# Kernel optimization log

Measured on AMD Instinct MI355X. Metric: run time of the kernel, lower is better.

## Reference

```python
import jax, jax.numpy as jnp
import numpy as np

NUM_CLASSES = 256
WEIGHT = 0.0005
EPS = 1e-12  # torch F.normalize eps


def setup_inputs() -> dict:
    key = jax.random.key(0)
    k1, k2 = jax.random.split(key)
    features = jax.random.normal(k1, (32768, 1024), dtype=jnp.float32)
    labels = jax.random.randint(k2, (32768,), 0, NUM_CLASSES, dtype=jnp.int32)
    return {"features": features, "labels": labels}


def _centroid_loss(features, labels):
    B, D = features.shape
    # row-wise L2 normalize (torch F.normalize: x / max(||x||, eps))
    norms = jnp.linalg.norm(features, axis=1, keepdims=True)
    f = features / jnp.maximum(norms, EPS)

    ones = jnp.ones((B,), f.dtype)
    counts = jax.ops.segment_sum(ones, labels, num_segments=NUM_CLASSES)  # [C]
    sums = jax.ops.segment_sum(f, labels, num_segments=NUM_CLASSES)       # [C, D]

    # rank of each sample within its class (order of first appearance),
    # matching the row order of features[class_mask] in the original loop
    onehot = jax.nn.one_hot(labels, NUM_CLASSES, dtype=jnp.int32)          # [B, C]
    rank = jnp.take_along_axis(jnp.cumsum(onehot, axis=0), labels[:, None].astype(jnp.int32), axis=1)[:, 0] - 1

    # idx_table[c, r] = global index of the r-th member of class c; sentinel B if none
    idx_table = jnp.full((NUM_CLASSES, B), B, dtype=jnp.int32)
    idx_table = idx_table.at[labels, rank].set(jnp.arange(B, dtype=jnp.int32))

    # NOTE: the original code indexes class_features with the GLOBAL index i
    # (arange(n_c) != i), i.e. it excludes the member of the class at position i,
    # and excludes nothing when i >= n_c. We reproduce that exactly.
    arange_b = jnp.arange(B)
    k = idx_table[labels, arange_b]            # class member at in-class position i (global i)
    valid_excl = k < B                          # exclusion only happens when i < class size
    excl_feat = jnp.where(valid_excl[:, None], f[jnp.where(valid_excl, k, 0)], 0.0)

    n_c = counts[labels]                        # class size per sample (float)
    denom = jnp.where(valid_excl, n_c - 1.0, n_c)
    denom = jnp.maximum(denom, 1.0)             # safe for masked-out singleton classes
    centroid = (sums[labels] - excl_feat) / denom[:, None]

    dist = jnp.mean((f - centroid) ** 2, axis=1)  # F.mse_loss(..., reduction='mean')
    contrib = jnp.where(n_c > 1.0, dist, 0.0)     # skip classes with <=1 sample
    return WEIGHT * jnp.sum(contrib) / B


def reference(features, labels):
    return _centroid_loss(features, labels)
```

## Files before the change

### kernel.cpp

```cpp
#include <hip/hip_runtime.h>

#define BN 32768
#define DN 1024
#define CN 256
#define RCAP 512
#define SUBS 8

__device__ __forceinline__ float dot4(float4 a, float4 b) {
    return a.x*b.x + a.y*b.y + a.z*b.z + a.w*b.w;
}

__global__ void __launch_bounds__(256) kc_compact(const int* __restrict__ labels,
                                                  int* __restrict__ idx,
                                                  int* __restrict__ counts) {
    __shared__ unsigned int packed[BN / 4];
    __shared__ int wcnt[4];
    const int c = blockIdx.x;
    const int t = threadIdx.x;

    for (int w = t; w < BN / 4; w += 256) {
        const int4 v = ((const int4*)labels)[w];
        packed[w] = (unsigned int)(v.x & 255)
                  | ((unsigned int)(v.y & 255) << 8)
                  | ((unsigned int)(v.z & 255) << 16)
                  | ((unsigned int)(v.w & 255) << 24);
    }
    __syncthreads();

    const int wave = t >> 6, lane = t & 63;
    const unsigned long long lt = (lane == 0) ? 0ull : (~0ull >> (64 - lane));
    const int ch0 = wave * 128, ch1 = ch0 + 128;

    int cnt = 0;
    for (int ch = ch0; ch < ch1; ++ch) {
        const int gi = ch * 64 + lane;
        const int lab = (packed[gi >> 2] >> ((gi & 3) * 8)) & 255;
        cnt += __popcll(__ballot(lab == c));
    }
    if (lane == 0) wcnt[wave] = cnt;
    __syncthreads();

    int base = 0;
    for (int w2 = 0; w2 < wave; ++w2) base += wcnt[w2];

    for (int ch = ch0; ch < ch1; ++ch) {
        const int gi = ch * 64 + lane;
        const int lab = (packed[gi >> 2] >> ((gi & 3) * 8)) & 255;
        const bool pred = (lab == c);
        const unsigned long long mask = __ballot(pred);
        if (pred) {
            const int pos = base + __popcll(mask & lt);
            if (pos < RCAP) idx[c * RCAP + pos] = gi;
        }
        base += __popcll(mask);
    }
    if (t == 0) counts[c] = wcnt[0] + wcnt[1] + wcnt[2] + wcnt[3];
}

__global__ void __launch_bounds__(256) k_rnorm(const float4* __restrict__ x4,
                                               float* __restrict__ rnorm) {
    const int wave = threadIdx.x >> 6;
    const int lane = threadIdx.x & 63;
    const int row = blockIdx.x * 4 + wave;
    const float4* base = x4 + (size_t)row * (DN / 4);
    const float4 v0 = base[lane];
    const float4 v1 = base[lane + 64];
    const float4 v2 = base[lane + 128];
    const float4 v3 = base[lane + 192];
    float ss = dot4(v0, v0) + dot4(v1, v1) + dot4(v2, v2) + dot4(v3, v3);
#pragma unroll
    for (int off = 32; off; off >>= 1) ss += __shfl_xor(ss, off, 64);
    if (lane == 0) rnorm[row] = 1.0f / fmaxf(sqrtf(ss), 1e-12f);
}

__global__ void __launch_bounds__(256) k_gather2(const float4* __restrict__ x4,
                                                 const int* __restrict__ idx,
                                                 const int* __restrict__ counts,
                                                 const float* __restrict__ rnorm,
                                                 float4* __restrict__ partials) {
    __shared__ int sic[RCAP];
    __shared__ float srn[RCAP];
    const int b = blockIdx.x;
    const int c = b >> 3;
    const int sub = b & 7;
    const int t = threadIdx.x;

    const int nn = min(counts[c], RCAP);
    const int nnpad = min((nn + 31) & ~31, RCAP);

    for (int i = t; i < nnpad; i += 256) {
        const int r = min(i, nn - 1);
        const int row = idx[c * RCAP + r];
        sic[i] = row;
        srn[i] = (i < nn) ? rnorm[row] : 0.0f;
    }
    __syncthreads();

    float4 acc = make_float4(0.f, 0.f, 0.f, 0.f);
    for (int base = sub * 4; base < nnpad; base += 32) {
        const int row0 = sic[base + 0], row1 = sic[base + 1];
        const int row2 = sic[base + 2], row3 = sic[base + 3];
        const float rn0 = srn[base + 0], rn1 = srn[base + 1];
        const float rn2 = srn[base + 2], rn3 = srn[base + 3];
        const float4 v0 = x4[(size_t)row0 * 256 + t];
        const float4 v1 = x4[(size_t)row1 * 256 + t];
        const float4 v2 = x4[(size_t)row2 * 256 + t];
        const float4 v3 = x4[(size_t)row3 * 256 + t];
        acc.x += v0.x * rn0; acc.y += v0.y * rn0; acc.z += v0.z * rn0; acc.w += v0.w * rn0;
        acc.x += v1.x * rn1; acc.y += v1.y * rn1; acc.z += v1.z * rn1; acc.w += v1.w * rn1;
        acc.x += v2.x * rn2; acc.y += v2.y * rn2; acc.z += v2.z * rn2; acc.w += v2.w * rn2;
        acc.x += v3.x * rn3; acc.y += v3.y * rn3; acc.z += v3.z * rn3; acc.w += v3.w * rn3;
    }
    partials[(size_t)b * 256 + t] = acc;
}

__global__ void __launch_bounds__(256) k_red(const float4* __restrict__ partials,
                                             const int* __restrict__ counts,
                                             float* __restrict__ sums,
                                             float* __restrict__ snorm2,
                                             float* __restrict__ acc) {
    __shared__ float wred[4];
    const int c = blockIdx.x;
    const int t = threadIdx.x;
    const int wave = t >> 6, lane = t & 63;

    float4 tot = make_float4(0.f, 0.f, 0.f, 0.f);
#pragma unroll
    for (int s = 0; s < SUBS; ++s) {
        const float4 p = partials[(size_t)(c * SUBS + s) * 256 + t];
        tot.x += p.x; tot.y += p.y; tot.z += p.z; tot.w += p.w;
    }
    ((float4*)sums)[(size_t)c * 256 + t] = tot;

    float d = dot4(tot, tot);
#pragma unroll
    for (int off = 32; off; off >>= 1) d += __shfl_xor(d, off, 64);
    if (lane == 0) wred[wave] = d;
    __syncthreads();
    if (t == 0) {
        const float s2 = wred[0] + wred[1] + wred[2] + wred[3];
        snorm2[c] = s2;
        const int n = counts[c];
        if (n > 1) {
            const float nf = (float)n;
            atomicAdd(acc, (nf - s2 / nf) * (1.0f / DN));
        }
    }
}

__global__ void __launch_bounds__(256) k_corr(const float4* __restrict__ x4,
                                              const int* __restrict__ labels,
                                              const int* __restrict__ counts,
                                              const int* __restrict__ idx,
                                              const float* __restrict__ rnorm,
                                              const float* __restrict__ sums,
                                              const float* __restrict__ snorm2,
                                              float* __restrict__ acc) {
    const int i = blockIdx.x;
    const int c = labels[i];
    const int n = counts[c];
    if (i >= n || n < 2 || i >= RCAP) return;
    const int k = idx[c * RCAP + i];
    const int t = threadIdx.x;

    const float4 xi = x4[(size_t)i * 256 + t];
    const float4 xk = x4[(size_t)k * 256 + t];
    const float4 s  = ((const float4*)sums)[(size_t)c * 256 + t];

    float d0 = dot4(xi, s);
    float d1 = dot4(xi, xk);
    float d2 = dot4(xk, s);
    float d3 = dot4(xk, xk);
#pragma unroll
    for (int off = 32; off; off >>= 1) {
        d0 += __shfl_xor(d0, off, 64);
        d1 += __shfl_xor(d1, off, 64);
        d2 += __shfl_xor(d2, off, 64);
        d3 += __shfl_xor(d3, off, 64);
    }
    __shared__ float4 wred[4];
    if ((t & 63) == 0) wred[t >> 6] = make_float4(d0, d1, d2, d3);
    __syncthreads();
    if (t == 0) {
        const float xiS  = wred[0].x + wred[1].x + wred[2].x + wred[3].x;
        const float xixk = wred[0].y + wred[1].y + wred[2].y + wred[3].y;
        const float xkS  = wred[0].z + wred[1].z + wred[2].z + wred[3].z;
        const float xkxk = wred[0].w + wred[1].w + wred[2].w + wred[3].w;
        const float rni = rnorm[i], rnk = rnorm[k], s2 = snorm2[c];
        const float fiS  = rni * xiS;
        const float fifk = rni * rnk * xixk;
        const float Sfk  = rnk * xkS;
        const float fk2  = rnk * rnk * xkxk;
        const float nf = (float)n;
        const float dd = nf - 1.0f;
        const float naive = -2.0f * fiS / nf + s2 / (nf * nf);
        const float corr  = -2.0f * (fiS - fifk) / dd + (s2 - 2.0f * Sfk + fk2) / (dd * dd);
        atomicAdd(acc, (corr - naive) * (1.0f / DN));
    }
}

__global__ void k_fin(const float* __restrict__ acc, float* __restrict__ out) {
    out[0] = (0.0005f / (float)BN) * acc[0];
}

extern "C" void kernel_launch(void* const* d_in, const int* in_sizes, int n_in,
                              void* d_out, int out_size, void* d_ws, size_t ws_size,
                              hipStream_t stream) {
    const float* features = (const float*)d_in[0];
    const int* labels = (const int*)d_in[1];
    float* out = (float*)d_out;

    char* ws = (char*)d_ws;
    float4* partials = (float4*)(ws + 0);
    float*  rnorm    = (float*)(ws + 8388608);
    float*  sums     = (float*)(ws + 8519680);
    int*    idx      = (int*)  (ws + 9568256);
    int*    counts   = (int*)  (ws + 10092544);
    float*  snorm2   = (float*)(ws + 10093568);
    float*  acc      = (float*)(ws + 10094592);

    const float4* x4 = (const float4*)features;

    hipMemsetAsync(acc, 0, sizeof(float), stream);
    kc_compact<<<CN, 256, 0, stream>>>(labels, idx, counts);
    k_rnorm<<<BN / 4, 256, 0, stream>>>(x4, rnorm);
    k_gather2<<<CN * SUBS, 256, 0, stream>>>(x4, idx, counts, rnorm, partials);
    k_red<<<CN, 256, 0, stream>>>(partials, counts, sums, snorm2, acc);
    k_corr<<<RCAP, 256, 0, stream>>>(x4, labels, counts, idx, rnorm, sums, snorm2, acc);
    k_fin<<<1, 1, 0, stream>>>(acc, out);
}
```

Baseline: 239.7 us.

## Replace per-class gather with streaming LDS-atomic scatter into class sums

Class sums are now built by streaming the feature matrix in row chunks and column slices. Each block accumulates normalized values into a per-class shared-memory table with LDS atomics, in place of gathering rows per class through the RCAP-capped index list. The reduction kernel sums the chunk partials in the new layout. The accumulator zeroing moves from a separate memset into the compaction kernel. This aims for fully streamed reads and better load balance, at the cost of LDS atomic contention, scalar strided loads and a 16 MB partials buffer.

```diff
diff --git a/kernel.cpp b/kernel.cpp
--- a/kernel.cpp
+++ b/kernel.cpp
@@ -4,7 +4,9 @@
 #define DN 1024
 #define CN 256
 #define RCAP 512
-#define SUBS 8
+#define NSLICE 16
+#define NCHUNK 16
+#define RPB (BN / NCHUNK)
 
 __device__ __forceinline__ float dot4(float4 a, float4 b) {
     return a.x*b.x + a.y*b.y + a.z*b.z + a.w*b.w;
@@ -12,7 +14,8 @@
 
 __global__ void __launch_bounds__(256) kc_compact(const int* __restrict__ labels,
                                                   int* __restrict__ idx,
-                                                  int* __restrict__ counts) {
+                                                  int* __restrict__ counts,
+                                                  float* __restrict__ acc) {
     __shared__ unsigned int packed[BN / 4];
     __shared__ int wcnt[4];
     const int c = blockIdx.x;
@@ -54,7 +57,10 @@
         }
         base += __popcll(mask);
     }
-    if (t == 0) counts[c] = wcnt[0] + wcnt[1] + wcnt[2] + wcnt[3];
+    if (t == 0) {
+        counts[c] = wcnt[0] + wcnt[1] + wcnt[2] + wcnt[3];
+        if (c == 0) *acc = 0.0f;
+    }
 }
 
 __global__ void __launch_bounds__(256) k_rnorm(const float4* __restrict__ x4,
@@ -73,48 +79,59 @@
     if (lane == 0) rnorm[row] = 1.0f / fmaxf(sqrtf(ss), 1e-12f);
 }
 
-__global__ void __launch_bounds__(256) k_gather2(const float4* __restrict__ x4,
-                                                 const int* __restrict__ idx,
-                                                 const int* __restrict__ counts,
-                                                 const float* __restrict__ rnorm,
-                                                 float4* __restrict__ partials) {
-    __shared__ int sic[RCAP];
-    __shared__ float srn[RCAP];
+__global__ void __launch_bounds__(1024) k_scatter(const float* __restrict__ x,
+                                                  const int* __restrict__ labels,
+                                                  const float* __restrict__ rnorm,
+                                                  float* __restrict__ partials) {
+    __shared__ float cacc[CN * 64];
+    __shared__ int   slab[RPB];
+    __shared__ float srn[RPB];
     const int b = blockIdx.x;
-    const int c = b >> 3;
-    const int sub = b & 7;
-    const int t = threadIdx.x;
-
-    const int nn = min(counts[c], RCAP);
-    const int nnpad = min((nn + 31) & ~31, RCAP);
-
-    for (int i = t; i < nnpad; i += 256) {
-        const int r = min(i, nn - 1);
-        const int row = idx[c * RCAP + r];
-        sic[i] = row;
-        srn[i] = (i < nn) ? rnorm[row] : 0.0f;
-    }
-    __syncthreads();
-
-    float4 acc = make_float4(0.f, 0.f, 0.f, 0.f);
-    for (int base = sub * 4; base < nnpad; base += 32) {
-        const int row0 = sic[base + 0], row1 = sic[base + 1];
-        const int row2 = sic[base + 2], row3 = sic[base + 3];
-        const float rn0 = srn[base + 0], rn1 = srn[base + 1];
-        const float rn2 = srn[base + 2], rn3 = srn[base + 3];
-        const float4 v0 = x4[(size_t)row0 * 256 + t];
-        const float4 v1 = x4[(size_t)row1 * 256 + t];
-        const float4 v2 = x4[(size_t)row2 * 256 + t];
-        const float4 v3 = x4[(size_t)row3 * 256 + t];
-        acc.x += v0.x * rn0; acc.y += v0.y * rn0; acc.z += v0.z * rn0; acc.w += v0.w * rn0;
-        acc.x += v1.x * rn1; acc.y += v1.y * rn1; acc.z += v1.z * rn1; acc.w += v1.w * rn1;
-        acc.x += v2.x * rn2; acc.y += v2.y * rn2; acc.z += v2.z * rn2; acc.w += v2.w * rn2;
-        acc.x += v3.x * rn3; acc.y += v3.y * rn3; acc.z += v3.z * rn3; acc.w += v3.w * rn3;
-    }
-    partials[(size_t)b * 256 + t] = acc;
-}
-
-__global__ void __launch_bounds__(256) k_red(const float4* __restrict__ partials,
+    const int slice = b & (NSLICE - 1);
+    const int chunk = b >> 4;
+    const int t = threadIdx.x;
+    const int wave = t >> 6, lane = t & 63;
+    const int r0 = chunk * RPB;
+
+    for (int i = t; i < CN * 64; i += 1024) cacc[i] = 0.0f;
+    for (int i = t; i < RPB; i += 1024) {
+        slab[i] = labels[r0 + i];
+        srn[i]  = rnorm[r0 + i];
+    }
+    __syncthreads();
+
+    const float* colbase = x + (size_t)r0 * DN + slice * 64 + lane;
+    const int wr0 = wave * (RPB / 16);
+    for (int i = 0; i < RPB / 16; i += 8) {
+        const int rr = wr0 + i;
+        const int   l0 = slab[rr + 0], l1 = slab[rr + 1], l2 = slab[rr + 2], l3 = slab[rr + 3];
+        const int   l4 = slab[rr + 4], l5 = slab[rr + 5], l6 = slab[rr + 6], l7 = slab[rr + 7];
+        const float r0f = srn[rr + 0], r1f = srn[rr + 1], r2f = srn[rr + 2], r3f = srn[rr + 3];
+        const float r4f = srn[rr + 4], r5f = srn[rr + 5], r6f = srn[rr + 6], r7f = srn[rr + 7];
+        const float v0 = colbase[(size_t)(rr + 0) * DN];
+        const float v1 = colbase[(size_t)(rr + 1) * DN];
+        const float v2 = colbase[(size_t)(rr + 2) * DN];
+        const float v3 = colbase[(size_t)(rr + 3) * DN];
+        const float v4 = colbase[(size_t)(rr + 4) * DN];
+        const float v5 = colbase[(size_t)(rr + 5) * DN];
+        const float v6 = colbase[(size_t)(rr + 6) * DN];
+        const float v7 = colbase[(size_t)(rr + 7) * DN];
+        atomicAdd(&cacc[l0 * 64 + lane], v0 * r0f);
+        atomicAdd(&cacc[l1 * 64 + lane], v1 * r1f);
+        atomicAdd(&cacc[l2 * 64 + lane], v2 * r2f);
+        atomicAdd(&cacc[l3 * 64 + lane], v3 * r3f);
+        atomicAdd(&cacc[l4 * 64 + lane], v4 * r4f);
+        atomicAdd(&cacc[l5 * 64 + lane], v5 * r5f);
+        atomicAdd(&cacc[l6 * 64 + lane], v6 * r6f);
+        atomicAdd(&cacc[l7 * 64 + lane], v7 * r7f);
+    }
+    __syncthreads();
+
+    float* pb = partials + (size_t)b * (CN * 64);
+    for (int i = t; i < CN * 64; i += 1024) pb[i] = cacc[i];
+}
+
+__global__ void __launch_bounds__(256) k_red(const float* __restrict__ partials,
                                              const int* __restrict__ counts,
                                              float* __restrict__ sums,
                                              float* __restrict__ snorm2,
@@ -124,15 +141,19 @@
     const int t = threadIdx.x;
     const int wave = t >> 6, lane = t & 63;
 
-    float4 tot = make_float4(0.f, 0.f, 0.f, 0.f);
-#pragma unroll
-    for (int s = 0; s < SUBS; ++s) {
-        const float4 p = partials[(size_t)(c * SUBS + s) * 256 + t];
-        tot.x += p.x; tot.y += p.y; tot.z += p.z; tot.w += p.w;
-    }
-    ((float4*)sums)[(size_t)c * 256 + t] = tot;
-
-    float d = dot4(tot, tot);
+    float d = 0.0f;
+#pragma unroll
+    for (int jj = 0; jj < 4; ++jj) {
+        const int j = t + jj * 256;
+        const int slice = j >> 6, col = j & 63;
+        float tot = 0.0f;
+#pragma unroll
+        for (int ch = 0; ch < NCHUNK; ++ch) {
+            tot += partials[(size_t)((ch * NSLICE + slice) * CN + c) * 64 + col];
+        }
+        sums[(size_t)c * DN + j] = tot;
+        d += tot * tot;
+    }
 #pragma unroll
     for (int off = 32; off; off >>= 1) d += __shfl_xor(d, off, 64);
     if (lane == 0) wred[wave] = d;
@@ -211,20 +232,19 @@
     float* out = (float*)d_out;
 
     char* ws = (char*)d_ws;
-    float4* partials = (float4*)(ws + 0);
-    float*  rnorm    = (float*)(ws + 8388608);
-    float*  sums     = (float*)(ws + 8519680);
-    int*    idx      = (int*)  (ws + 9568256);
-    int*    counts   = (int*)  (ws + 10092544);
-    float*  snorm2   = (float*)(ws + 10093568);
-    float*  acc      = (float*)(ws + 10094592);
+    float* partials = (float*)(ws + 0);
+    float* rnorm    = (float*)(ws + 16777216);
+    float* sums     = (float*)(ws + 16908288);
+    int*   idx      = (int*)  (ws + 17956864);
+    int*   counts   = (int*)  (ws + 18481152);
+    float* snorm2   = (float*)(ws + 18482176);
+    float* acc      = (float*)(ws + 18483200);
 
     const float4* x4 = (const float4*)features;
 
-    hipMemsetAsync(acc, 0, sizeof(float), stream);
-    kc_compact<<<CN, 256, 0, stream>>>(labels, idx, counts);
+    kc_compact<<<CN, 256, 0, stream>>>(labels, idx, counts, acc);
     k_rnorm<<<BN / 4, 256, 0, stream>>>(x4, rnorm);
-    k_gather2<<<CN * SUBS, 256, 0, stream>>>(x4, idx, counts, rnorm, partials);
+    k_scatter<<<NCHUNK * NSLICE, 1024, 0, stream>>>(features, labels, rnorm, partials);
     k_red<<<CN, 256, 0, stream>>>(partials, counts, sums, snorm2, acc);
     k_corr<<<RCAP, 256, 0, stream>>>(x4, labels, counts, idx, rnorm, sums, snorm2, acc);
     k_fin<<<1, 1, 0, stream>>>(acc, out);
```

After: 397.3 us. +65.7%, slower.
